# Kernel optimization log

Measured on AMD Instinct MI355X. Metric: run time of the kernel, lower is better.

The kernel has to match this reference:

```python
import jax, jax.numpy as jnp
import numpy as np

H, HKV, D, HID = 32, 8, 128, 4096
L, CTX, S = 64, 64, 8192
T = CTX + L
HALF = D // 2
EPS = 1e-6
WP = 4096


def setup_inputs() -> dict:
    key = jax.random.key(0)
    ks = jax.random.split(key, 16)
    f = jnp.float32
    w = 0.02
    return {
        "x": jax.random.normal(ks[0], (1, L, HID), f),
        "x_ctx": jax.random.normal(ks[1], (1, CTX, HID), f),
        "cos_q": jax.random.uniform(ks[2], (1, 1, L, HALF), f, -1.0, 1.0),
        "sin_q": jax.random.uniform(ks[3], (1, 1, L, HALF), f, -1.0, 1.0),
        "cos_k": jax.random.uniform(ks[4], (1, 1, T, HALF), f, -1.0, 1.0),
        "sin_k": jax.random.uniform(ks[5], (1, 1, T, HALF), f, -1.0, 1.0),
        "cache_K_in": jax.random.normal(ks[6], (1, HKV, S, D), f),
        "cache_V_in": jax.random.normal(ks[7], (1, HKV, S, D), f),
        "causal_mask": jnp.ones((1, 1, L, WP + T), dtype=bool),
        "Wq": jax.random.normal(ks[8], (HID, H * D), f) * w,
        "Wk": jax.random.normal(ks[9], (HID, HKV * D), f) * w,
        "Wv": jax.random.normal(ks[10], (HID, HKV * D), f) * w,
        "Wo": jax.random.normal(ks[11], (H * D, HID), f) * w,
        "q_norm_w": jnp.ones((D,), f),
        "k_norm_w": jnp.ones((D,), f),
        "write_pos": WP,
        "rotate": 0,
    }


def _rmsnorm(x, w):
    # normalize over head_dim (last axis)
    var = jnp.mean(x * x, axis=-1, keepdims=True)
    return x * jax.lax.rsqrt(var + EPS) * w


def _rope(x, cos, sin):
    # x: (B, H, T, D); cos/sin: (1, 1, T, HALF) -- rotate-half convention
    x1, x2 = x[..., :HALF], x[..., HALF:]
    return jnp.concatenate([x1 * cos - x2 * sin, x2 * cos + x1 * sin], axis=-1)


def reference(x, x_ctx, cos_q, sin_q, cos_k, sin_k, cache_K_in, cache_V_in,
              causal_mask, Wq, Wk, Wv, Wo, q_norm_w, k_norm_w, write_pos, rotate):
    c = jnp.concatenate([x_ctx, x], axis=1)                  # (1, T, HID)
    q = (x @ Wq).reshape(1, L, H, D)
    k = (c @ Wk).reshape(1, T, HKV, D)
    v = (c @ Wv).reshape(1, T, HKV, D)
    q = _rmsnorm(q, q_norm_w).transpose(0, 2, 1, 3)          # (1, H, L, D)
    k = _rmsnorm(k, k_norm_w).transpose(0, 2, 1, 3)          # (1, HKV, T, D)
    v = v.transpose(0, 2, 1, 3)                               # (1, HKV, T, D)
    q = _rope(q, cos_q, sin_q)
    k = _rope(k, cos_k, sin_k)

    if rotate:  # static Python branch (rotate is a compile-time constant)
        attend_K = jnp.concatenate([cache_K_in[:, :, T:S], k], axis=2)
        attend_V = jnp.concatenate([cache_V_in[:, :, T:S], v], axis=2)
    elif write_pos == 0:
        attend_K, attend_V = k, v
    else:
        attend_K = jnp.concatenate([cache_K_in[:, :, :write_pos], k], axis=2)
        attend_V = jnp.concatenate([cache_V_in[:, :, :write_pos], v], axis=2)

    rep = H // HKV
    scale = jnp.float32(D) ** -0.5
    qg = q.reshape(1, HKV, rep, L, D)
    # grouped attention: broadcast KV heads inline instead of materializing expand
    scores = jnp.einsum('bgrld,bgad->bgrla', qg, attend_K) * scale
    scores = jnp.where(causal_mask[:, :, None], scores, -jnp.inf)  # (1,1,1,L,A) bcast
    probs = jax.nn.softmax(scores, axis=-1)
    o = jnp.einsum('bgrla,bgad->bgrld', probs, attend_V)     # (1, HKV, rep, L, D)
    o = o.reshape(1, H, L, D).transpose(0, 2, 1, 3).reshape(1, L, H * D)
    return (o @ Wo, k, v)
```

## Files before the change

kernel.cpp:

```cpp
#include <hip/hip_runtime.h>

typedef unsigned short u16;
typedef __bf16 bf16x8 __attribute__((ext_vector_type(8)));
typedef float f32x4 __attribute__((ext_vector_type(4)));
typedef u16 u16x8 __attribute__((ext_vector_type(8)));

#define NSPLIT 22
#define KSPLIT 4
#define KC 1024
#define NKT 16
#define OSPLIT 8
#define SCALE_Q 0.08838834764831843f

__device__ __forceinline__ u16 f2bf(float f) {
    unsigned u = __builtin_bit_cast(unsigned, f);
    u += 0x7fff + ((u >> 16) & 1);
    return (u16)(u >> 16);
}
__device__ __forceinline__ float bf2f(u16 h) {
    unsigned u = ((unsigned)h) << 16;
    return __builtin_bit_cast(float, u);
}
__device__ __forceinline__ f32x4 mfma16(bf16x8 a, bf16x8 b, f32x4 c) {
    return __builtin_amdgcn_mfma_f32_16x16x32_bf16(a, b, c, 0, 0, 0);
}

__global__ __launch_bounds__(256)
void k_prep(const float* __restrict__ x, const float* __restrict__ xctx,
            u16* __restrict__ fragA)
{
    int tid = blockIdx.x * 256 + threadIdx.x;
    int row = tid >> 9;
    int kc = tid & 511;
    int k0 = kc << 3;
    const float* src = (row < 64) ? (xctx + (size_t)row * 4096)
                                  : (x + (size_t)(row - 64) * 4096);
    f32x4 v0 = *(const f32x4*)&src[k0];
    f32x4 v1 = *(const f32x4*)&src[k0 + 4];
    u16x8 o;
    o[0] = f2bf(v0[0]); o[1] = f2bf(v0[1]); o[2] = f2bf(v0[2]); o[3] = f2bf(v0[3]);
    o[4] = f2bf(v1[0]); o[5] = f2bf(v1[1]); o[6] = f2bf(v1[2]); o[7] = f2bf(v1[3]);
    int ks32 = k0 >> 5;
    int lg = (k0 >> 3) & 3;
    int rt = row >> 4;
    int l = lg * 16 + (row & 15);
    *(u16x8*)&fragA[(((size_t)ks32 * 8 + rt) * 64 + l) * 8] = o;
}

__global__ __launch_bounds__(256)
void k_qkv(const u16* __restrict__ fragA,
           const float* __restrict__ Wq, const float* __restrict__ Wk,
           const float* __restrict__ Wv, float* __restrict__ part)
{
    const int col0 = blockIdx.x * 32;
    const int ksp = blockIdx.y;
    const int ks0 = ksp * KC;
    const float* W; int ldw, cbase, mat;
    if (col0 < 4096)      { W = Wq; ldw = 4096; cbase = col0;        mat = 0; }
    else if (col0 < 5120) { W = Wk; ldw = 1024; cbase = col0 - 4096; mat = 1; }
    else                  { W = Wv; ldw = 1024; cbase = col0 - 5120; mat = 2; }
    const bool full = (mat != 0);
    const int rowbase = full ? 0 : 64;

    __shared__ __align__(16) u16 Bs[32 * 64];

    const int t = threadIdx.x;
    const int w = t >> 6, l = t & 63;
    const int lm = l & 15, lg = l >> 4;

    const int bk = (t >> 3) << 1;
    const int bn4 = (t & 7) << 2;

    f32x4 pb[2];
    f32x4 acc[2][2] = {};

    const int rt0 = full ? (w * 2) : (4 + w);

    #define QKV_BLOAD(kt_)                                                     \
    {                                                                          \
        const int kg = ks0 + (kt_) * 64;                                       \
        pb[0] = *(const f32x4*)&W[(size_t)(kg + bk) * ldw + cbase + bn4];      \
        pb[1] = *(const f32x4*)&W[(size_t)(kg + bk + 1) * ldw + cbase + bn4];  \
    }

    #define QKV_BSTORE()                                                       \
    {                                                                          \
        _Pragma("unroll")                                                      \
        for (int j = 0; j < 4; j++) {                                          \
            int n = bn4 + j;                                                   \
            int idx = n * 64 + (bk ^ (((n >> 1) & 7) << 3));                   \
            ushort2 v2; v2.x = f2bf(pb[0][j]); v2.y = f2bf(pb[1][j]);          \
            *(ushort2*)&Bs[idx] = v2;                                          \
        }                                                                      \
    }

    QKV_BLOAD(0);
    #pragma unroll 1
    for (int kt = 0; kt < NKT; kt++) {
        if (kt) __syncthreads();
        QKV_BSTORE();
        __syncthreads();
        if (kt + 1 < NKT) QKV_BLOAD(kt + 1);
        const int ks32b = (ks0 >> 5) + kt * 2;
        #pragma unroll
        for (int ks = 0; ks < 2; ks++) {
            const int koff = ks * 32 + lg * 8;
            bf16x8 a0 = *(const bf16x8*)
                &fragA[(((size_t)(ks32b + ks) * 8 + rt0) * 64 + l) * 8];
            bf16x8 bfr[2];
            #pragma unroll
            for (int nt = 0; nt < 2; nt++) {
                int n = nt * 16 + lm;
                bfr[nt] = *(const bf16x8*)&Bs[n * 64 + (koff ^ (((n >> 1) & 7) << 3))];
            }
            acc[0][0] = mfma16(a0, bfr[0], acc[0][0]);
            acc[0][1] = mfma16(a0, bfr[1], acc[0][1]);
            if (full) {
                bf16x8 a1 = *(const bf16x8*)
                    &fragA[(((size_t)(ks32b + ks) * 8 + rt0 + 1) * 64 + l) * 8];
                acc[1][0] = mfma16(a1, bfr[0], acc[1][0]);
                acc[1][1] = mfma16(a1, bfr[1], acc[1][1]);
            }
        }
    }

    const int wrows = full ? 32 : 16;
    const int mts = full ? 2 : 1;
    #pragma unroll
    for (int mt = 0; mt < 2; mt++) {
        if (mt >= mts) break;
        #pragma unroll
        for (int nt = 0; nt < 2; nt++)
            #pragma unroll
            for (int r = 0; r < 4; r++) {
                int grow = rowbase + w * wrows + mt * 16 + lg * 4 + r;
                part[((size_t)ksp * 128 + grow) * 6144 + col0 + nt * 16 + lm] =
                    acc[mt][nt][r];
            }
    }
    #undef QKV_BLOAD
    #undef QKV_BSTORE
}

__global__ __launch_bounds__(256)
void k_normrope(const float* __restrict__ part,
                const float* __restrict__ cosq, const float* __restrict__ sinq,
                const float* __restrict__ cosk, const float* __restrict__ sink,
                const float* __restrict__ qnw, const float* __restrict__ knw,
                u16* __restrict__ qb, u16* __restrict__ kb,
                float* __restrict__ outk, float* __restrict__ outv,
                u16* __restrict__ vbw)
{
    int wid = blockIdx.x * 4 + (threadIdx.x >> 6);
    int lane = threadIdx.x & 63;
    if (wid < 2048) {
        int h = wid >> 6, lq = wid & 63;
        size_t ro = (size_t)(64 + lq) * 6144 + h * 128;
        float x1 = 0.f, x2 = 0.f;
        #pragma unroll
        for (int s = 0; s < KSPLIT; s++) {
            x1 += part[(size_t)s * 786432 + ro + lane];
            x2 += part[(size_t)s * 786432 + ro + lane + 64];
        }
        float ss = x1 * x1 + x2 * x2;
        #pragma unroll
        for (int off = 32; off; off >>= 1) ss += __shfl_xor(ss, off);
        float rms = rsqrtf(ss * (1.0f / 128.0f) + 1e-6f);
        float a = x1 * rms * qnw[lane];
        float b = x2 * rms * qnw[lane + 64];
        float c = cosq[lq * 64 + lane], s = sinq[lq * 64 + lane];
        u16* qo = qb + ((size_t)h * 64 + lq) * 128;
        qo[lane]      = f2bf((a * c - b * s) * SCALE_Q);
        qo[lane + 64] = f2bf((b * c + a * s) * SCALE_Q);
    } else if (wid < 3072) {
        int rr = wid - 2048;
        int kh = rr >> 7, tt = rr & 127;
        size_t ro = (size_t)tt * 6144 + 4096 + kh * 128;
        float x1 = 0.f, x2 = 0.f;
        #pragma unroll
        for (int s = 0; s < KSPLIT; s++) {
            x1 += part[(size_t)s * 786432 + ro + lane];
            x2 += part[(size_t)s * 786432 + ro + lane + 64];
        }
        float ss = x1 * x1 + x2 * x2;
        #pragma unroll
        for (int off = 32; off; off >>= 1) ss += __shfl_xor(ss, off);
        float rms = rsqrtf(ss * (1.0f / 128.0f) + 1e-6f);
        float a = x1 * rms * knw[lane];
        float b = x2 * rms * knw[lane + 64];
        float c = cosk[tt * 64 + lane], s = sink[tt * 64 + lane];
        float o1 = a * c - b * s, o2 = b * c + a * s;
        size_t oi = ((size_t)kh * 128 + tt) * 128;
        outk[oi + lane] = o1; outk[oi + lane + 64] = o2;
        kb[oi + lane] = f2bf(o1); kb[oi + lane + 64] = f2bf(o2);
    } else {
        int rr = wid - 3072;
        int kh = rr >> 7, tt = rr & 127;
        size_t ro = (size_t)tt * 6144 + 5120 + kh * 128;
        float v1 = 0.f, v2 = 0.f;
        #pragma unroll
        for (int s = 0; s < KSPLIT; s++) {
            v1 += part[(size_t)s * 786432 + ro + lane];
            v2 += part[(size_t)s * 786432 + ro + lane + 64];
        }
        size_t oi = ((size_t)kh * 128 + tt) * 128;
        outv[oi + lane] = v1; outv[oi + lane + 64] = v2;
        vbw[oi + lane] = f2bf(v1); vbw[oi + lane + 64] = f2bf(v2);
    }
}

__global__ __launch_bounds__(256)
void k_attn(const u16* __restrict__ qb, const u16* __restrict__ kbw,
            const u16* __restrict__ vbw,
            const float* __restrict__ cacheK, const float* __restrict__ cacheV,
            u16* __restrict__ opart, float* __restrict__ lpart)
{
    const int split = blockIdx.x;
    const int kh = blockIdx.y;
    const int t = threadIdx.x;
    const int w = t >> 6, l = t & 63;
    const int lm = l & 15, lg = l >> 4;

    __shared__ __align__(16) u16 Ks[64][136];
    __shared__ __align__(16) u16 Vs[128][72];
    __shared__ __align__(16) u16 Ps[4][64][40];

    const u16* qh = qb + ((size_t)(kh * 4 + w) * 64) * 128;
    bf16x8 aq[4][4];
    #pragma unroll
    for (int mt = 0; mt < 4; mt++)
        #pragma unroll
        for (int ks = 0; ks < 4; ks++)
            aq[mt][ks] = *(const bf16x8*)&qh[(size_t)(mt * 16 + lm) * 128 + ks * 32 + lg * 8];

    f32x4 accO[4][8] = {};
    float lacc[4][4] = {};
    const size_t khK = (size_t)kh * 8192 * 128;

    for (int kbi = 0; kbi < 3; kbi++) {
        const int key0 = split * 192 + kbi * 64;
        __syncthreads();
        #pragma unroll
        for (int it = 0; it < 8; it++) {
            int fidx = it * 256 + t;
            int row = fidx >> 5;
            int d4 = (fidx & 31) << 2;
            int key = key0 + row;
            if (key < 4096) {
                float4 kv = *(const float4*)&cacheK[khK + (size_t)key * 128 + d4];
                ushort4 sv; sv.x = f2bf(kv.x); sv.y = f2bf(kv.y);
                sv.z = f2bf(kv.z); sv.w = f2bf(kv.w);
                *(ushort4*)&Ks[row][d4] = sv;
                float4 vv = *(const float4*)&cacheV[khK + (size_t)key * 128 + d4];
                Vs[d4 + 0][row] = f2bf(vv.x);
                Vs[d4 + 1][row] = f2bf(vv.y);
                Vs[d4 + 2][row] = f2bf(vv.z);
                Vs[d4 + 3][row] = f2bf(vv.w);
            } else {
                size_t nb = ((size_t)kh * 128 + (key - 4096)) * 128 + d4;
                ushort4 kv = *(const ushort4*)&kbw[nb];
                *(ushort4*)&Ks[row][d4] = kv;
                ushort4 vv = *(const ushort4*)&vbw[nb];
                Vs[d4 + 0][row] = vv.x;
                Vs[d4 + 1][row] = vv.y;
                Vs[d4 + 2][row] = vv.z;
                Vs[d4 + 3][row] = vv.w;
            }
        }
        __syncthreads();

        f32x4 sa[4][4] = {};
        #pragma unroll
        for (int ks = 0; ks < 4; ks++) {
            bf16x8 bk[4];
            #pragma unroll
            for (int nt = 0; nt < 4; nt++)
                bk[nt] = *(const bf16x8*)&Ks[nt * 16 + lm][ks * 32 + lg * 8];
            #pragma unroll
            for (int mt = 0; mt < 4; mt++)
                #pragma unroll
                for (int nt = 0; nt < 4; nt++)
                    sa[mt][nt] = mfma16(aq[mt][ks], bk[nt], sa[mt][nt]);
        }

        #pragma unroll
        for (int half = 0; half < 2; half++) {
            __syncthreads();
            #pragma unroll
            for (int mt = 0; mt < 4; mt++)
                #pragma unroll
                for (int nt2 = 0; nt2 < 2; nt2++)
                    #pragma unroll
                    for (int r = 0; r < 4; r++) {
                        float e = __expf(sa[mt][half * 2 + nt2][r]);
                        lacc[mt][r] += e;
                        Ps[w][mt * 16 + lg * 4 + r][nt2 * 16 + lm] = f2bf(e);
                    }
            __syncthreads();
            bf16x8 pa[4];
            #pragma unroll
            for (int mt = 0; mt < 4; mt++)
                pa[mt] = *(const bf16x8*)&Ps[w][mt * 16 + lm][lg * 8];
            #pragma unroll
            for (int dt = 0; dt < 8; dt++) {
                bf16x8 vb8 = *(const bf16x8*)&Vs[dt * 16 + lm][half * 32 + lg * 8];
                #pragma unroll
                for (int mt = 0; mt < 4; mt++)
                    accO[mt][dt] = mfma16(pa[mt], vb8, accO[mt][dt]);
            }
        }
    }

    #pragma unroll
    for (int mt = 0; mt < 4; mt++)
        #pragma unroll
        for (int r = 0; r < 4; r++) {
            float v = lacc[mt][r];
            v += __shfl_xor(v, 1);
            v += __shfl_xor(v, 2);
            v += __shfl_xor(v, 4);
            v += __shfl_xor(v, 8);
            lacc[mt][r] = v;
        }

    const size_t base = (((size_t)kh * NSPLIT + split) * 4 + w) * 64;
    if (lm == 0) {
        #pragma unroll
        for (int mt = 0; mt < 4; mt++)
            #pragma unroll
            for (int r = 0; r < 4; r++)
                lpart[base + mt * 16 + lg * 4 + r] = lacc[mt][r];
    }
    #pragma unroll
    for (int mt = 0; mt < 4; mt++)
        #pragma unroll
        for (int dt = 0; dt < 8; dt++)
            #pragma unroll
            for (int r = 0; r < 4; r++)
                opart[(base + mt * 16 + lg * 4 + r) * 128 + dt * 16 + lm] =
                    f2bf(accO[mt][dt][r]);
}

__global__ __launch_bounds__(256)
void k_combine(const u16* __restrict__ opart, const float* __restrict__ lpart,
               u16* __restrict__ obf)
{
    int idx = blockIdx.x * 256 + threadIdx.x;
    int lq = idx >> 12;
    int col = idx & 4095;
    int h = col >> 7, d = col & 127;
    int kh = h >> 2, rep = h & 3;
    float os = 0.f, ls = 0.f;
    #pragma unroll 2
    for (int s = 0; s < NSPLIT; s++) {
        size_t b = (((size_t)kh * NSPLIT + s) * 4 + rep) * 64 + lq;
        os += bf2f(opart[b * 128 + d]);
        ls += lpart[b];
    }
    obf[idx] = f2bf(os / ls);
}

__global__ __launch_bounds__(256)
void k_oproj(const u16* __restrict__ obf, const float* __restrict__ Wo,
             float* __restrict__ parto)
{
    const int col0 = blockIdx.x * 32;
    const int osp = blockIdx.y;
    const int ks0 = osp * (4096 / OSPLIT);

    __shared__ __align__(16) u16 As[64][72];
    __shared__ __align__(16) u16 Bs[32 * 64];

    const int t = threadIdx.x;
    const int w = t >> 6, l = t & 63;
    const int lm = l & 15, lg = l >> 4;

    const int arow = t >> 3;
    const int ac8 = (t & 7) << 3;
    const int bk = (t >> 3) << 1;
    const int bn4 = (t & 7) << 2;

    u16x8 pa[2]; f32x4 pb[2];
    f32x4 acc[2] = {};

    #define OP_LOAD(kt_)                                                       \
    {                                                                          \
        const int kg = ks0 + (kt_) * 64;                                       \
        pa[0] = *(const u16x8*)&obf[(size_t)arow * 4096 + kg + ac8];           \
        pa[1] = *(const u16x8*)&obf[(size_t)(arow + 32) * 4096 + kg + ac8];    \
        pb[0] = *(const f32x4*)&Wo[(size_t)(kg + bk) * 4096 + col0 + bn4];     \
        pb[1] = *(const f32x4*)&Wo[(size_t)(kg + bk + 1) * 4096 + col0 + bn4]; \
    }

    #define OP_STORE()                                                         \
    {                                                                          \
        *(u16x8*)&As[arow][ac8] = pa[0];                                       \
        *(u16x8*)&As[arow + 32][ac8] = pa[1];                                  \
        _Pragma("unroll")                                                      \
        for (int j = 0; j < 4; j++) {                                          \
            int n = bn4 + j;                                                   \
            int idx = n * 64 + (bk ^ (((n >> 1) & 7) << 3));                   \
            ushort2 v2; v2.x = f2bf(pb[0][j]); v2.y = f2bf(pb[1][j]);          \
            *(ushort2*)&Bs[idx] = v2;                                          \
        }                                                                      \
    }

    OP_LOAD(0);
    #pragma unroll 1
    for (int kt = 0; kt < 4096 / OSPLIT / 64; kt++) {
        if (kt) __syncthreads();
        OP_STORE();
        __syncthreads();
        if (kt + 1 < 4096 / OSPLIT / 64) OP_LOAD(kt + 1);
        #pragma unroll
        for (int ks = 0; ks < 2; ks++) {
            const int koff = ks * 32 + lg * 8;
            bf16x8 a0 = *(const bf16x8*)&As[w * 16 + lm][koff];
            #pragma unroll
            for (int nt = 0; nt < 2; nt++) {
                int n = nt * 16 + lm;
                bf16x8 b = *(const bf16x8*)&Bs[n * 64 + (koff ^ (((n >> 1) & 7) << 3))];
                acc[nt] = mfma16(a0, b, acc[nt]);
            }
        }
    }
    #pragma unroll
    for (int nt = 0; nt < 2; nt++)
        #pragma unroll
        for (int r = 0; r < 4; r++)
            parto[((size_t)osp * 64 + w * 16 + lg * 4 + r) * 4096 +
                  col0 + nt * 16 + lm] = acc[nt][r];
    #undef OP_LOAD
    #undef OP_STORE
}

__global__ __launch_bounds__(256)
void k_osum(const float* __restrict__ parto, float* __restrict__ out0)
{
    int idx = blockIdx.x * 256 + threadIdx.x;
    float s = 0.f;
    #pragma unroll
    for (int o = 0; o < OSPLIT; o++)
        s += parto[(size_t)o * 262144 + idx];
    out0[idx] = s;
}

extern "C" void kernel_launch(void* const* d_in, const int* in_sizes, int n_in,
                              void* d_out, int out_size, void* d_ws, size_t ws_size,
                              hipStream_t stream)
{
    (void)in_sizes; (void)n_in; (void)out_size; (void)ws_size;
    const float* x      = (const float*)d_in[0];
    const float* xctx   = (const float*)d_in[1];
    const float* cosq   = (const float*)d_in[2];
    const float* sinq   = (const float*)d_in[3];
    const float* cosk   = (const float*)d_in[4];
    const float* sink   = (const float*)d_in[5];
    const float* cacheK = (const float*)d_in[6];
    const float* cacheV = (const float*)d_in[7];
    const float* Wq     = (const float*)d_in[9];
    const float* Wk     = (const float*)d_in[10];
    const float* Wv     = (const float*)d_in[11];
    const float* Wo     = (const float*)d_in[12];
    const float* qnw    = (const float*)d_in[13];
    const float* knw    = (const float*)d_in[14];

    float* out0 = (float*)d_out;
    float* out1 = out0 + 262144;
    float* out2 = out1 + 131072;

    char* ws = (char*)d_ws;
    float* part  = (float*)(ws + 0);
    u16*   opart = (u16*)(ws + 0);
    float* lpart = (float*)(ws + 11534336);
    float* parto = (float*)(ws + 0);
    u16*   fragA = (u16*)(ws + 12582912);
    u16*   qb    = (u16*)(ws + 12582912);
    u16*   kb    = (u16*)(ws + 13107200);
    u16*   vb    = (u16*)(ws + 13369344);
    u16*   obf   = (u16*)(ws + 13631488);

    k_prep<<<256, 256, 0, stream>>>(x, xctx, fragA);
    k_qkv<<<dim3(192, KSPLIT), 256, 0, stream>>>(fragA, Wq, Wk, Wv, part);
    k_normrope<<<1024, 256, 0, stream>>>(part, cosq, sinq, cosk, sink,
                                         qnw, knw, qb, kb, out1, out2, vb);
    k_attn<<<dim3(NSPLIT, 8), 256, 0, stream>>>(qb, kb, vb, cacheK, cacheV,
                                                opart, lpart);
    k_combine<<<1024, 256, 0, stream>>>(opart, lpart, obf);
    k_oproj<<<dim3(128, OSPLIT), 256, 0, stream>>>(obf, Wo, parto);
    k_osum<<<1024, 256, 0, stream>>>(parto, out0);
}
```

Measured before the change: 94.48 us.

## Narrow QKV GEMM column tiles and split attention into more key blocks

The QKV projection kernel now gives each block 16 output columns instead of 32, which doubles the grid to 384x4 blocks and halves the per-block B tile and its accumulators. Attention is templated on split count and keys per block. When the workspace is large enough it launches 66 splits of 64 keys each instead of 22 splits of 192 keys, and the workspace offsets are shifted to fit the larger partial buffers. The aim is to fill more compute units in both kernels. The cost is more partial results for the combine kernel to read and reduce, and more redundant per-block Q fragment loads.

Result: slower. 119.6 us (+26.6%).

```diff
diff --git a/kernel.cpp b/kernel.cpp
--- a/kernel.cpp
+++ b/kernel.cpp
@@ -5,7 +5,6 @@
 typedef float f32x4 __attribute__((ext_vector_type(4)));
 typedef u16 u16x8 __attribute__((ext_vector_type(8)));
 
-#define NSPLIT 22
 #define KSPLIT 4
 #define KC 1024
 #define NKT 16
@@ -52,7 +51,7 @@
            const float* __restrict__ Wq, const float* __restrict__ Wk,
            const float* __restrict__ Wv, float* __restrict__ part)
 {
-    const int col0 = blockIdx.x * 32;
+    const int col0 = blockIdx.x * 16;
     const int ksp = blockIdx.y;
     const int ks0 = ksp * KC;
     const float* W; int ldw, cbase, mat;
@@ -62,35 +61,29 @@
     const bool full = (mat != 0);
     const int rowbase = full ? 0 : 64;
 
-    __shared__ __align__(16) u16 Bs[32 * 64];
+    __shared__ __align__(16) u16 Bs[16 * 64];
 
     const int t = threadIdx.x;
     const int w = t >> 6, l = t & 63;
     const int lm = l & 15, lg = l >> 4;
 
-    const int bk = (t >> 3) << 1;
-    const int bn4 = (t & 7) << 2;
-
-    f32x4 pb[2];
-    f32x4 acc[2][2] = {};
+    const int bkk = t >> 2;
+    const int bn4 = (t & 3) << 2;
+
+    f32x4 pb;
+    f32x4 acc[2] = {};
 
     const int rt0 = full ? (w * 2) : (4 + w);
 
     #define QKV_BLOAD(kt_)                                                     \
-    {                                                                          \
-        const int kg = ks0 + (kt_) * 64;                                       \
-        pb[0] = *(const f32x4*)&W[(size_t)(kg + bk) * ldw + cbase + bn4];      \
-        pb[1] = *(const f32x4*)&W[(size_t)(kg + bk + 1) * ldw + cbase + bn4];  \
-    }
+        pb = *(const f32x4*)&W[(size_t)(ks0 + (kt_) * 64 + bkk) * ldw + cbase + bn4];
 
     #define QKV_BSTORE()                                                       \
     {                                                                          \
         _Pragma("unroll")                                                      \
         for (int j = 0; j < 4; j++) {                                          \
             int n = bn4 + j;                                                   \
-            int idx = n * 64 + (bk ^ (((n >> 1) & 7) << 3));                   \
-            ushort2 v2; v2.x = f2bf(pb[0][j]); v2.y = f2bf(pb[1][j]);          \
-            *(ushort2*)&Bs[idx] = v2;                                          \
+            Bs[n * 64 + (bkk ^ (((n >> 1) & 7) << 3))] = f2bf(pb[j]);          \
         }                                                                      \
     }
 
@@ -105,21 +98,14 @@
         #pragma unroll
         for (int ks = 0; ks < 2; ks++) {
             const int koff = ks * 32 + lg * 8;
+            bf16x8 b = *(const bf16x8*)&Bs[lm * 64 + (koff ^ (((lm >> 1) & 7) << 3))];
             bf16x8 a0 = *(const bf16x8*)
                 &fragA[(((size_t)(ks32b + ks) * 8 + rt0) * 64 + l) * 8];
-            bf16x8 bfr[2];
-            #pragma unroll
-            for (int nt = 0; nt < 2; nt++) {
-                int n = nt * 16 + lm;
-                bfr[nt] = *(const bf16x8*)&Bs[n * 64 + (koff ^ (((n >> 1) & 7) << 3))];
-            }
-            acc[0][0] = mfma16(a0, bfr[0], acc[0][0]);
-            acc[0][1] = mfma16(a0, bfr[1], acc[0][1]);
+            acc[0] = mfma16(a0, b, acc[0]);
             if (full) {
                 bf16x8 a1 = *(const bf16x8*)
                     &fragA[(((size_t)(ks32b + ks) * 8 + rt0 + 1) * 64 + l) * 8];
-                acc[1][0] = mfma16(a1, bfr[0], acc[1][0]);
-                acc[1][1] = mfma16(a1, bfr[1], acc[1][1]);
+                acc[1] = mfma16(a1, b, acc[1]);
             }
         }
     }
@@ -130,13 +116,10 @@
     for (int mt = 0; mt < 2; mt++) {
         if (mt >= mts) break;
         #pragma unroll
-        for (int nt = 0; nt < 2; nt++)
-            #pragma unroll
-            for (int r = 0; r < 4; r++) {
-                int grow = rowbase + w * wrows + mt * 16 + lg * 4 + r;
-                part[((size_t)ksp * 128 + grow) * 6144 + col0 + nt * 16 + lm] =
-                    acc[mt][nt][r];
-            }
+        for (int r = 0; r < 4; r++) {
+            int grow = rowbase + w * wrows + mt * 16 + lg * 4 + r;
+            part[((size_t)ksp * 128 + grow) * 6144 + col0 + lm] = acc[mt][r];
+        }
     }
     #undef QKV_BLOAD
     #undef QKV_BSTORE
@@ -209,6 +192,7 @@
     }
 }
 
+template<int NSP, int NBLK>
 __global__ __launch_bounds__(256)
 void k_attn(const u16* __restrict__ qb, const u16* __restrict__ kbw,
             const u16* __restrict__ vbw,
@@ -237,8 +221,8 @@
     float lacc[4][4] = {};
     const size_t khK = (size_t)kh * 8192 * 128;
 
-    for (int kbi = 0; kbi < 3; kbi++) {
-        const int key0 = split * 192 + kbi * 64;
+    for (int kbi = 0; kbi < NBLK; kbi++) {
+        const int key0 = split * (64 * NBLK) + kbi * 64;
         __syncthreads();
         #pragma unroll
         for (int it = 0; it < 8; it++) {
@@ -323,7 +307,7 @@
             lacc[mt][r] = v;
         }
 
-    const size_t base = (((size_t)kh * NSPLIT + split) * 4 + w) * 64;
+    const size_t base = (((size_t)kh * NSP + split) * 4 + w) * 64;
     if (lm == 0) {
         #pragma unroll
         for (int mt = 0; mt < 4; mt++)
@@ -341,6 +325,7 @@
                     f2bf(accO[mt][dt][r]);
 }
 
+template<int NSP>
 __global__ __launch_bounds__(256)
 void k_combine(const u16* __restrict__ opart, const float* __restrict__ lpart,
                u16* __restrict__ obf)
@@ -351,9 +336,9 @@
     int h = col >> 7, d = col & 127;
     int kh = h >> 2, rep = h & 3;
     float os = 0.f, ls = 0.f;
-    #pragma unroll 2
-    for (int s = 0; s < NSPLIT; s++) {
-        size_t b = (((size_t)kh * NSPLIT + s) * 4 + rep) * 64 + lq;
+    #pragma unroll 4
+    for (int s = 0; s < NSP; s++) {
+        size_t b = (((size_t)kh * NSP + s) * 4 + rep) * 64 + lq;
         os += bf2f(opart[b * 128 + d]);
         ls += lpart[b];
     }
@@ -449,7 +434,7 @@
                               void* d_out, int out_size, void* d_ws, size_t ws_size,
                               hipStream_t stream)
 {
-    (void)in_sizes; (void)n_in; (void)out_size; (void)ws_size;
+    (void)in_sizes; (void)n_in; (void)out_size;
     const float* x      = (const float*)d_in[0];
     const float* xctx   = (const float*)d_in[1];
     const float* cosq   = (const float*)d_in[2];
@@ -469,24 +454,34 @@
     float* out1 = out0 + 262144;
     float* out2 = out1 + 131072;
 
+    const bool big = (ws_size >= 36716544ull);
     char* ws = (char*)d_ws;
+    const size_t lpart_off = big ? 34603008ull : 11534336ull;
+    const size_t regB      = big ? 35143680ull : 12582912ull;
+
     float* part  = (float*)(ws + 0);
     u16*   opart = (u16*)(ws + 0);
-    float* lpart = (float*)(ws + 11534336);
+    float* lpart = (float*)(ws + lpart_off);
     float* parto = (float*)(ws + 0);
-    u16*   fragA = (u16*)(ws + 12582912);
-    u16*   qb    = (u16*)(ws + 12582912);
-    u16*   kb    = (u16*)(ws + 13107200);
-    u16*   vb    = (u16*)(ws + 13369344);
-    u16*   obf   = (u16*)(ws + 13631488);
+    u16*   fragA = (u16*)(ws + regB);
+    u16*   qb    = (u16*)(ws + regB);
+    u16*   kb    = (u16*)(ws + regB + 524288);
+    u16*   vb    = (u16*)(ws + regB + 786432);
+    u16*   obf   = (u16*)(ws + regB + 1048576);
 
     k_prep<<<256, 256, 0, stream>>>(x, xctx, fragA);
-    k_qkv<<<dim3(192, KSPLIT), 256, 0, stream>>>(fragA, Wq, Wk, Wv, part);
+    k_qkv<<<dim3(384, KSPLIT), 256, 0, stream>>>(fragA, Wq, Wk, Wv, part);
     k_normrope<<<1024, 256, 0, stream>>>(part, cosq, sinq, cosk, sink,
                                          qnw, knw, qb, kb, out1, out2, vb);
-    k_attn<<<dim3(NSPLIT, 8), 256, 0, stream>>>(qb, kb, vb, cacheK, cacheV,
-                                                opart, lpart);
-    k_combine<<<1024, 256, 0, stream>>>(opart, lpart, obf);
+    if (big) {
+        k_attn<66, 1><<<dim3(66, 8), 256, 0, stream>>>(qb, kb, vb, cacheK, cacheV,
+                                                       opart, lpart);
+        k_combine<66><<<1024, 256, 0, stream>>>(opart, lpart, obf);
+    } else {
+        k_attn<22, 3><<<dim3(22, 8), 256, 0, stream>>>(qb, kb, vb, cacheK, cacheV,
+                                                       opart, lpart);
+        k_combine<22><<<1024, 256, 0, stream>>>(opart, lpart, obf);
+    }
     k_oproj<<<dim3(128, OSPLIT), 256, 0, stream>>>(obf, Wo, parto);
     k_osum<<<1024, 256, 0, stream>>>(parto, out0);
 }
```
